# Performance work log

Measured on AMD Instinct MI355X. Metric: run time of the kernel, lower is better.

Reference implementation:

```python
import jax, jax.numpy as jnp
import numpy as np

B, D, T, H, C = 256, 128, 512, 256, 10


def _xavier(key, shape):
    fan_in, fan_out = shape[0], shape[1]
    std = jnp.sqrt(2.0 / (fan_in + fan_out))
    return jax.random.normal(key, shape, dtype=jnp.float32) * std


def setup_inputs() -> dict:
    key = jax.random.key(0)
    ks = jax.random.split(key, 10)
    return {
        "x": jax.random.normal(ks[0], (B, D, T), dtype=jnp.float32),
        "W_gx": _xavier(ks[1], (D, H)),
        "W_ix": _xavier(ks[2], (D, H)),
        "W_fx": _xavier(ks[3], (D, H)),
        "W_ox": _xavier(ks[4], (D, H)),
        "W_gh": _xavier(ks[5], (H, H)),
        "W_ih": _xavier(ks[6], (H, H)),
        "W_fh": _xavier(ks[7], (H, H)),
        "W_oh": _xavier(ks[8], (H, H)),
        "b_g": jnp.zeros((H,), jnp.float32),
        "b_i": jnp.zeros((H,), jnp.float32),
        "b_f": jnp.zeros((H,), jnp.float32),
        "b_o": jnp.zeros((H,), jnp.float32),
        "W_ph": _xavier(ks[9], (H, C)),
        "b_p": jnp.zeros((C,), jnp.float32),
    }


def reference(x, W_gx, W_ix, W_fx, W_ox, W_gh, W_ih, W_fh, W_oh,
              b_g, b_i, b_f, b_o, W_ph, b_p):
    # x: [B, D, T] -> time-major [T, B, D]
    xs = jnp.transpose(x, (2, 0, 1))
    # Precompute all input-to-gate projections in one big GEMM per gate
    # (same math as per-step x_ @ W_*x, just batched over time).
    gx = jnp.einsum('tbd,dh->tbh', xs, W_gx) + b_g
    ix = jnp.einsum('tbd,dh->tbh', xs, W_ix) + b_i
    fx = jnp.einsum('tbd,dh->tbh', xs, W_fx) + b_f
    ox = jnp.einsum('tbd,dh->tbh', xs, W_ox) + b_o

    h0 = jnp.zeros((x.shape[0], W_gh.shape[0]), x.dtype)
    c0 = jnp.zeros_like(h0)

    def step(carry, inp):
        h, c = carry
        gx_t, ix_t, fx_t, ox_t = inp
        g = jnp.tanh(gx_t + h @ W_gh)
        i = jax.nn.sigmoid(ix_t + h @ W_ih)
        f = jax.nn.sigmoid(fx_t + h @ W_fh)
        o = jax.nn.sigmoid(ox_t + h @ W_oh)
        c = g * i + c * f
        h = jnp.tanh(c) * o
        return (h, c), None

    (h, c), _ = jax.lax.scan(step, (h0, c0), (gx, ix, fx, ox))
    return h @ W_ph + b_p
```

## Files before the change

kernel.cpp:

```cpp
#include <hip/hip_runtime.h>
#include <hip/hip_bf16.h>
#include <cstdint>

#define B_ 256
#define D_ 128
#define T_ 512
#define H_ 256
#define C_ 10

using f32x4 = __attribute__((ext_vector_type(4))) float;
using s16x8 = __attribute__((ext_vector_type(8))) short;

__device__ __forceinline__ unsigned short f2bf(float f) {
    union { float f; uint32_t u; } a; a.f = f;
    uint32_t u = a.u;
    uint32_t r = (u + 0x7fffu + ((u >> 16) & 1u)) >> 16;
    return (unsigned short)r;
}

__device__ __forceinline__ float sigm(float v) { return 1.0f / (1.0f + __expf(-v)); }

__global__ void xt_kernel(const float* __restrict__ x, unsigned short* __restrict__ xt) {
    __shared__ unsigned short tile[128][66];
    const int b  = blockIdx.x >> 3;
    const int t0 = (blockIdx.x & 7) << 6;
    const int tid = threadIdx.x;
    const int j  = tid & 63;
    const int dq = tid >> 6;

#pragma unroll
    for (int it = 0; it < 32; ++it) {
        int d = it * 4 + dq;
        tile[d][j] = f2bf(x[(size_t)(b * D_ + d) * T_ + t0 + j]);
    }
    __syncthreads();

    uint32_t* xt32 = (uint32_t*)xt;
#pragma unroll
    for (int it = 0; it < 16; ++it) {
        int tl = it * 4 + dq;
        int dp = j;
        uint32_t lo = tile[2 * dp][tl];
        uint32_t hi = tile[2 * dp + 1][tl];
        xt32[(size_t)((t0 + tl) * B_ + b) * (D_ / 2) + dp] = lo | (hi << 16);
    }
}

__global__ void __launch_bounds__(256) lstm_kernel(
    const float* __restrict__ Wgx, const float* __restrict__ Wix,
    const float* __restrict__ Wfx, const float* __restrict__ Wox,
    const float* __restrict__ Wgh, const float* __restrict__ Wih,
    const float* __restrict__ Wfh, const float* __restrict__ Woh,
    const float* __restrict__ bg,  const float* __restrict__ bi,
    const float* __restrict__ bf2, const float* __restrict__ bo,
    const unsigned short* __restrict__ xt,
    uint64_t* __restrict__ hbuf,
    int* __restrict__ flags,
    float* __restrict__ hfin)
{
    __shared__ __align__(16) unsigned short Wh_s[4][16][264];
    __shared__ __align__(16) unsigned short Wx_s[4][16][136];
    __shared__ __align__(16) unsigned short h_s[16][264];
    __shared__ __align__(16) unsigned short x_s[16][136];
    __shared__ float pre_s[4][16][17];
    __shared__ float bias_s[4][16];

    const int tid  = threadIdx.x;
    const int bc   = blockIdx.x & 15;
    const int hc   = blockIdx.x >> 4;
    const int wave = tid >> 6;
    const int lane = tid & 63;
    const int mrow = lane & 15;
    const int quad = lane >> 4;

    const float* Wh[4] = {Wgh, Wih, Wfh, Woh};
    const float* Wx[4] = {Wgx, Wix, Wfx, Wox};
    const float* bias[4] = {bg, bi, bf2, bo};

#pragma unroll
    for (int g = 0; g < 4; ++g) {
        for (int it = 0; it < 16; ++it) {
            int idx = it * 256 + tid;
            int k = idx >> 4, c = idx & 15;
            Wh_s[g][c][k] = f2bf(Wh[g][(size_t)k * H_ + hc * 16 + c]);
        }
        for (int it = 0; it < 8; ++it) {
            int idx = it * 256 + tid;
            int k = idx >> 4, c = idx & 15;
            Wx_s[g][c][k] = f2bf(Wx[g][(size_t)k * H_ + hc * 16 + c]);
        }
    }
    if (tid < 64) bias_s[tid >> 4][tid & 15] = bias[tid >> 4][hc * 16 + (tid & 15)];
    __syncthreads();

    const int b_l = tid >> 4;
    const int u_l = tid & 15;
    float c_st = 0.0f, h_st = 0.0f;

    uint4 xv = *(const uint4*)(xt + ((size_t)(0 * B_ + bc * 16 + b_l) * D_ + u_l * 8));

    for (int t = 0; t < T_; ++t) {
        *(uint4*)&x_s[b_l][u_l * 8] = xv;

        if (t > 0 && tid < 16) {
            while (__hip_atomic_load(&flags[bc * 16 + tid], __ATOMIC_RELAXED,
                                     __HIP_MEMORY_SCOPE_AGENT) < t) {
                __builtin_amdgcn_s_sleep(1);
            }
        }
        __syncthreads();

        if (t + 1 < T_)
            xv = *(const uint4*)(xt + ((size_t)((t + 1) * B_ + bc * 16 + b_l) * D_ + u_l * 8));

        uint64_t hv[4];
        if (t > 0) {
            const uint64_t* src = hbuf + (size_t)((t - 1) & 1) * B_ * (H_ / 4);
#pragma unroll
            for (int i = 0; i < 4; ++i) {
                int idx = i * 256 + tid;
                int row = idx >> 6, kp = idx & 63;
                hv[i] = __hip_atomic_load(&src[(size_t)(bc * 16 + row) * (H_ / 4) + kp],
                                          __ATOMIC_RELAXED, __HIP_MEMORY_SCOPE_AGENT);
            }
        }

        f32x4 accx = {0.f, 0.f, 0.f, 0.f};
#pragma unroll
        for (int kk = 0; kk < 4; ++kk) {
            s16x8 a  = *(const s16x8*)&x_s[mrow][kk * 32 + quad * 8];
            s16x8 bb = *(const s16x8*)&Wx_s[wave][mrow][kk * 32 + quad * 8];
            accx = __builtin_amdgcn_mfma_f32_16x16x32_bf16(a, bb, accx, 0, 0, 0);
        }

        if (t > 0) {
#pragma unroll
            for (int i = 0; i < 4; ++i) {
                int idx = i * 256 + tid;
                int row = idx >> 6, kp = idx & 63;
                *(uint64_t*)&h_s[row][kp * 4] = hv[i];
            }
        }
        __syncthreads();

        f32x4 acc0 = {0.f, 0.f, 0.f, 0.f};
        f32x4 acc1 = {0.f, 0.f, 0.f, 0.f};
        if (t > 0) {
#pragma unroll
            for (int j = 0; j < 4; ++j) {
                s16x8 a  = *(const s16x8*)&h_s[mrow][(2 * j) * 32 + quad * 8];
                s16x8 bb = *(const s16x8*)&Wh_s[wave][mrow][(2 * j) * 32 + quad * 8];
                acc0 = __builtin_amdgcn_mfma_f32_16x16x32_bf16(a, bb, acc0, 0, 0, 0);
                s16x8 a2  = *(const s16x8*)&h_s[mrow][(2 * j + 1) * 32 + quad * 8];
                s16x8 bb2 = *(const s16x8*)&Wh_s[wave][mrow][(2 * j + 1) * 32 + quad * 8];
                acc1 = __builtin_amdgcn_mfma_f32_16x16x32_bf16(a2, bb2, acc1, 0, 0, 0);
            }
        }

#pragma unroll
        for (int r = 0; r < 4; ++r)
            pre_s[wave][quad * 4 + r][mrow] = accx[r] + acc0[r] + acc1[r];
        __syncthreads();

        float pg = pre_s[0][b_l][u_l] + bias_s[0][u_l];
        float pi = pre_s[1][b_l][u_l] + bias_s[1][u_l];
        float pf = pre_s[2][b_l][u_l] + bias_s[2][u_l];
        float po = pre_s[3][b_l][u_l] + bias_s[3][u_l];
        float gg = 2.0f * sigm(2.0f * pg) - 1.0f;
        float ii = sigm(pi), ff = sigm(pf), oo = sigm(po);
        c_st = gg * ii + c_st * ff;
        float th = 2.0f * sigm(2.0f * c_st) - 1.0f;
        h_st = th * oo;

        uint32_t hb = f2bf(h_st);
        uint32_t p = hb | ((uint32_t)__shfl_down((int)hb, 1, 64) << 16);
        uint32_t q = (uint32_t)__shfl_down((int)p, 2, 64);
        if ((tid & 3) == 0) {
            uint64_t val = ((uint64_t)q << 32) | (uint64_t)p;
            uint64_t* dst = hbuf + (size_t)(t & 1) * B_ * (H_ / 4);
            __hip_atomic_store(&dst[(size_t)(bc * 16 + b_l) * (H_ / 4) + hc * 4 + (u_l >> 2)],
                               val, __ATOMIC_RELAXED, __HIP_MEMORY_SCOPE_AGENT);
        }
        __syncthreads();
        if (tid == 0)
            __hip_atomic_store(&flags[bc * 16 + hc], t + 1, __ATOMIC_RELAXED,
                               __HIP_MEMORY_SCOPE_AGENT);
    }

    hfin[(size_t)(bc * 16 + b_l) * H_ + hc * 16 + u_l] = h_st;
}

__global__ void proj_kernel(const float* __restrict__ hfin, const float* __restrict__ Wph,
                            const float* __restrict__ bp, float* __restrict__ out) {
    int gid = blockIdx.x * 256 + threadIdx.x;
    if (gid >= B_ * C_) return;
    int b = gid / C_, cc = gid % C_;
    float acc = bp[cc];
#pragma unroll 8
    for (int u = 0; u < H_; ++u)
        acc += hfin[(size_t)b * H_ + u] * Wph[(size_t)u * C_ + cc];
    out[gid] = acc;
}

extern "C" void kernel_launch(void* const* d_in, const int* in_sizes, int n_in,
                              void* d_out, int out_size, void* d_ws, size_t ws_size,
                              hipStream_t stream) {
    const float* x   = (const float*)d_in[0];
    const float* Wgx = (const float*)d_in[1];
    const float* Wix = (const float*)d_in[2];
    const float* Wfx = (const float*)d_in[3];
    const float* Wox = (const float*)d_in[4];
    const float* Wgh = (const float*)d_in[5];
    const float* Wih = (const float*)d_in[6];
    const float* Wfh = (const float*)d_in[7];
    const float* Woh = (const float*)d_in[8];
    const float* bg  = (const float*)d_in[9];
    const float* bi  = (const float*)d_in[10];
    const float* bf2 = (const float*)d_in[11];
    const float* bo  = (const float*)d_in[12];
    const float* Wph = (const float*)d_in[13];
    const float* bp  = (const float*)d_in[14];

    char* ws = (char*)d_ws;
    int*            flags = (int*)ws;
    uint64_t*       hbuf  = (uint64_t*)(ws + 1024);
    float*          hfin  = (float*)(ws + 1024 + 2 * B_ * (H_ / 4) * 8);
    unsigned short* xt    = (unsigned short*)(ws + 1024 + 2 * B_ * (H_ / 4) * 8 + B_ * H_ * 4);

    hipMemsetAsync(flags, 0, 16 * 16 * sizeof(int), stream);

    xt_kernel<<<B_ * (T_ / 64), 256, 0, stream>>>(x, xt);

    lstm_kernel<<<256, 256, 0, stream>>>(Wgx, Wix, Wfx, Wox, Wgh, Wih, Wfh, Woh,
                                         bg, bi, bf2, bo, xt, hbuf, flags, hfin);

    proj_kernel<<<(B_ * C_ + 255) / 256, 256, 0, stream>>>(hfin, Wph, bp, (float*)d_out);
}
```

Baseline: 1.197 ms.

## Tag hidden-state words with step index, drop flag polling, fuse projection

Each 64-bit hidden-state word now carries two bf16 values plus the producing time step in its upper half. Consumers spin directly on the data loads until every tag matches. This replaces the separate flag spin-wait, the follow-up data load and the extra barrier with a single round trip per step. Plain barriers become explicit lgkmcnt-wait plus s_barrier, and the final output projection is folded into the recurrent kernel via shuffle reductions and atomicAdd on a zeroed output. In exchange, each step moves twice as many hbuf words, and the sum order of the projection is no longer deterministic.

After: 1.596 ms. 33.3% more time.

```diff
diff --git a/kernel.cpp b/kernel.cpp
--- a/kernel.cpp
+++ b/kernel.cpp
@@ -19,6 +19,10 @@
 }
 
 __device__ __forceinline__ float sigm(float v) { return 1.0f / (1.0f + __expf(-v)); }
+
+__device__ __forceinline__ void bar_lds() {
+    asm volatile("s_waitcnt lgkmcnt(0)\n\ts_barrier" ::: "memory");
+}
 
 __global__ void xt_kernel(const float* __restrict__ x, unsigned short* __restrict__ xt) {
     __shared__ unsigned short tile[128][66];
@@ -55,8 +59,8 @@
     const float* __restrict__ bf2, const float* __restrict__ bo,
     const unsigned short* __restrict__ xt,
     uint64_t* __restrict__ hbuf,
-    int* __restrict__ flags,
-    float* __restrict__ hfin)
+    const float* __restrict__ Wph, const float* __restrict__ bp,
+    float* __restrict__ out)
 {
     __shared__ __align__(16) unsigned short Wh_s[4][16][264];
     __shared__ __align__(16) unsigned short Wx_s[4][16][136];
@@ -97,33 +101,28 @@
     const int u_l = tid & 15;
     float c_st = 0.0f, h_st = 0.0f;
 
-    uint4 xv = *(const uint4*)(xt + ((size_t)(0 * B_ + bc * 16 + b_l) * D_ + u_l * 8));
+    const int kp    = tid & 127;
+    const int rbase = tid >> 7;
+
+    uint4 xv = *(const uint4*)(xt + ((size_t)(bc * 16 + b_l) * D_ + u_l * 8));
 
     for (int t = 0; t < T_; ++t) {
+        uint64_t hv[8];
+        const uint64_t* src = hbuf + (size_t)((t - 1) & 1) * (B_ * (H_ / 2));
+        if (t > 0) {
+#pragma unroll
+            for (int i = 0; i < 8; ++i) {
+                int row = i * 2 + rbase;
+                hv[i] = __hip_atomic_load(&src[(size_t)(bc * 16 + row) * (H_ / 2) + kp],
+                                          __ATOMIC_RELAXED, __HIP_MEMORY_SCOPE_AGENT);
+            }
+        }
+
         *(uint4*)&x_s[b_l][u_l * 8] = xv;
-
-        if (t > 0 && tid < 16) {
-            while (__hip_atomic_load(&flags[bc * 16 + tid], __ATOMIC_RELAXED,
-                                     __HIP_MEMORY_SCOPE_AGENT) < t) {
-                __builtin_amdgcn_s_sleep(1);
-            }
-        }
-        __syncthreads();
+        bar_lds();
 
         if (t + 1 < T_)
             xv = *(const uint4*)(xt + ((size_t)((t + 1) * B_ + bc * 16 + b_l) * D_ + u_l * 8));
-
-        uint64_t hv[4];
-        if (t > 0) {
-            const uint64_t* src = hbuf + (size_t)((t - 1) & 1) * B_ * (H_ / 4);
-#pragma unroll
-            for (int i = 0; i < 4; ++i) {
-                int idx = i * 256 + tid;
-                int row = idx >> 6, kp = idx & 63;
-                hv[i] = __hip_atomic_load(&src[(size_t)(bc * 16 + row) * (H_ / 4) + kp],
-                                          __ATOMIC_RELAXED, __HIP_MEMORY_SCOPE_AGENT);
-            }
-        }
 
         f32x4 accx = {0.f, 0.f, 0.f, 0.f};
 #pragma unroll
@@ -134,14 +133,27 @@
         }
 
         if (t > 0) {
-#pragma unroll
-            for (int i = 0; i < 4; ++i) {
-                int idx = i * 256 + tid;
-                int row = idx >> 6, kp = idx & 63;
-                *(uint64_t*)&h_s[row][kp * 4] = hv[i];
-            }
-        }
-        __syncthreads();
+            const uint32_t want = (uint32_t)(t - 1);
+            while (true) {
+                bool ok = true;
+#pragma unroll
+                for (int i = 0; i < 8; ++i)
+                    ok &= ((uint32_t)(hv[i] >> 32) == want);
+                if (ok) break;
+#pragma unroll
+                for (int i = 0; i < 8; ++i) {
+                    int row = i * 2 + rbase;
+                    hv[i] = __hip_atomic_load(&src[(size_t)(bc * 16 + row) * (H_ / 2) + kp],
+                                              __ATOMIC_RELAXED, __HIP_MEMORY_SCOPE_AGENT);
+                }
+            }
+#pragma unroll
+            for (int i = 0; i < 8; ++i) {
+                int row = i * 2 + rbase;
+                *(uint32_t*)&h_s[row][2 * kp] = (uint32_t)hv[i];
+            }
+        }
+        bar_lds();
 
         f32x4 acc0 = {0.f, 0.f, 0.f, 0.f};
         f32x4 acc1 = {0.f, 0.f, 0.f, 0.f};
@@ -160,7 +172,7 @@
 #pragma unroll
         for (int r = 0; r < 4; ++r)
             pre_s[wave][quad * 4 + r][mrow] = accx[r] + acc0[r] + acc1[r];
-        __syncthreads();
+        bar_lds();
 
         float pg = pre_s[0][b_l][u_l] + bias_s[0][u_l];
         float pi = pre_s[1][b_l][u_l] + bias_s[1][u_l];
@@ -174,32 +186,32 @@
 
         uint32_t hb = f2bf(h_st);
         uint32_t p = hb | ((uint32_t)__shfl_down((int)hb, 1, 64) << 16);
-        uint32_t q = (uint32_t)__shfl_down((int)p, 2, 64);
-        if ((tid & 3) == 0) {
-            uint64_t val = ((uint64_t)q << 32) | (uint64_t)p;
-            uint64_t* dst = hbuf + (size_t)(t & 1) * B_ * (H_ / 4);
-            __hip_atomic_store(&dst[(size_t)(bc * 16 + b_l) * (H_ / 4) + hc * 4 + (u_l >> 2)],
+        if ((tid & 1) == 0) {
+            uint64_t val = (uint64_t)p | ((uint64_t)(uint32_t)t << 32);
+            uint64_t* dst = hbuf + (size_t)(t & 1) * (B_ * (H_ / 2));
+            __hip_atomic_store(&dst[(size_t)(bc * 16 + b_l) * (H_ / 2) + hc * 8 + (u_l >> 1)],
                                val, __ATOMIC_RELAXED, __HIP_MEMORY_SCOPE_AGENT);
         }
-        __syncthreads();
-        if (tid == 0)
-            __hip_atomic_store(&flags[bc * 16 + hc], t + 1, __ATOMIC_RELAXED,
-                               __HIP_MEMORY_SCOPE_AGENT);
-    }
-
-    hfin[(size_t)(bc * 16 + b_l) * H_ + hc * 16 + u_l] = h_st;
-}
-
-__global__ void proj_kernel(const float* __restrict__ hfin, const float* __restrict__ Wph,
-                            const float* __restrict__ bp, float* __restrict__ out) {
-    int gid = blockIdx.x * 256 + threadIdx.x;
-    if (gid >= B_ * C_) return;
-    int b = gid / C_, cc = gid % C_;
-    float acc = bp[cc];
-#pragma unroll 8
-    for (int u = 0; u < H_; ++u)
-        acc += hfin[(size_t)b * H_ + u] * Wph[(size_t)u * C_ + cc];
-    out[gid] = acc;
+    }
+
+    {
+        const int urow = hc * 16 + u_l;
+        float wrow[C_];
+#pragma unroll
+        for (int c = 0; c < C_; ++c) wrow[c] = Wph[(size_t)urow * C_ + c];
+#pragma unroll
+        for (int c = 0; c < C_; ++c) {
+            float v = h_st * wrow[c];
+            v += __shfl_xor(v, 1, 64);
+            v += __shfl_xor(v, 2, 64);
+            v += __shfl_xor(v, 4, 64);
+            v += __shfl_xor(v, 8, 64);
+            if (u_l == 0) {
+                if (hc == 0) v += bp[c];
+                atomicAdd(&out[(size_t)(bc * 16 + b_l) * C_ + c], v);
+            }
+        }
+    }
 }
 
 extern "C" void kernel_launch(void* const* d_in, const int* in_sizes, int n_in,
@@ -222,17 +234,14 @@
     const float* bp  = (const float*)d_in[14];
 
     char* ws = (char*)d_ws;
-    int*            flags = (int*)ws;
-    uint64_t*       hbuf  = (uint64_t*)(ws + 1024);
-    float*          hfin  = (float*)(ws + 1024 + 2 * B_ * (H_ / 4) * 8);
-    unsigned short* xt    = (unsigned short*)(ws + 1024 + 2 * B_ * (H_ / 4) * 8 + B_ * H_ * 4);
-
-    hipMemsetAsync(flags, 0, 16 * 16 * sizeof(int), stream);
+    uint64_t*       hbuf = (uint64_t*)ws;
+    unsigned short* xt   = (unsigned short*)(ws + 2 * B_ * (H_ / 2) * 8);
+
+    hipMemsetAsync(d_out, 0, B_ * C_ * sizeof(float), stream);
 
     xt_kernel<<<B_ * (T_ / 64), 256, 0, stream>>>(x, xt);
 
     lstm_kernel<<<256, 256, 0, stream>>>(Wgx, Wix, Wfx, Wox, Wgh, Wih, Wfh, Woh,
-                                         bg, bi, bf2, bo, xt, hbuf, flags, hfin);
-
-    proj_kernel<<<(B_ * C_ + 255) / 256, 256, 0, stream>>>(hfin, Wph, bp, (float*)d_out);
-}
+                                         bg, bi, bf2, bo, xt, hbuf,
+                                         Wph, bp, (float*)d_out);
+}
```
